# Kernel tuning notes

Hardware: AMD Instinct MI355X
Metric: run time of the kernel (lower is better)

The kernel has to match this reference:

```python
import jax, jax.numpy as jnp
import numpy as np

HIDDEN = 4096
INTER = 11008
BATCH, SEQ = 2, 2048


def _ternary(key, shape):
    # BitNet b1.58 ternary weights in {-1, 0, +1}
    return jax.random.randint(key, shape, -1, 2).astype(jnp.float32)


def setup_inputs() -> dict:
    key = jax.random.key(0)
    kx, kg, ku, kd = jax.random.split(key, 4)
    x = jax.random.normal(kx, (BATCH, SEQ, HIDDEN), dtype=jnp.float32)
    gate_w = _ternary(kg, (INTER, HIDDEN))
    up_w = _ternary(ku, (INTER, HIDDEN))
    down_w = _ternary(kd, (HIDDEN, INTER))
    # per-tensor absmean scales (dequant factors)
    gate_scale = jnp.float32(0.02)
    up_scale = jnp.float32(0.02)
    down_scale = jnp.float32(0.02)
    return {"x": x, "gate_w": gate_w, "up_w": up_w, "down_w": down_w,
            "gate_scale": gate_scale, "up_scale": up_scale, "down_scale": down_scale}


def reference(x, gate_w, up_w, down_w, gate_scale, up_scale, down_scale):
    # QuantizedLinear: y = (x @ W_q^T) * scale, W_q ternary, bias=False
    gate = jnp.einsum('bsh,ih->bsi', x, gate_w) * gate_scale
    up = jnp.einsum('bsh,ih->bsi', x, up_w) * up_scale
    inter = jax.nn.silu(gate) * up  # SwiGLU
    out = jnp.einsum('bsi,hi->bsh', inter, down_w) * down_scale
    return out
```

## Files before the change

### kernel.cpp

```cpp
#include <hip/hip_runtime.h>


typedef short short8 __attribute__((ext_vector_type(8)));
typedef float f32x4 __attribute__((ext_vector_type(4)));
typedef float fvec4 __attribute__((ext_vector_type(4)));
typedef unsigned short usvec4 __attribute__((ext_vector_type(4)));

__device__ __forceinline__ unsigned short f2bf(float f) {
    unsigned int u = __float_as_uint(f);
    u += 0x7FFFu + ((u >> 16) & 1u);
    return (unsigned short)(u >> 16);
}

__global__ void cvt_f32_bf16(const fvec4* __restrict__ src,
                             usvec4* __restrict__ dst, long n4) {
    long i = (long)blockIdx.x * blockDim.x + threadIdx.x;
    if (i < n4) {
        fvec4 v = __builtin_nontemporal_load(src + i);
        usvec4 o;
        o.x = f2bf(v.x); o.y = f2bf(v.y); o.z = f2bf(v.z); o.w = f2bf(v.w);
        dst[i] = o;
    }
}

__global__ void cvt2_f32_bf16_ilv(const fvec4* __restrict__ s0,
                                  const fvec4* __restrict__ s1,
                                  usvec4* __restrict__ d, long n4) {
    long i = (long)blockIdx.x * blockDim.x + threadIdx.x;
    if (i < n4) {
        long j = i >> 10;
        long c = i & 1023;
        long Rg = ((j & ~15L) << 1) | (j & 15);
        fvec4 a = __builtin_nontemporal_load(s0 + i);
        fvec4 b = __builtin_nontemporal_load(s1 + i);
        usvec4 oa, ob;
        oa.x = f2bf(a.x); oa.y = f2bf(a.y); oa.z = f2bf(a.z); oa.w = f2bf(a.w);
        ob.x = f2bf(b.x); ob.y = f2bf(b.y); ob.z = f2bf(b.z); ob.w = f2bf(b.w);
        d[Rg * 1024 + c] = oa;
        d[(Rg + 16) * 1024 + c] = ob;
    }
}

#define GLOBAL_TO_LDS(gp, lp)                                                  \
    __builtin_amdgcn_global_load_lds(                                          \
        (__attribute__((address_space(1))) const void*)(gp),                   \
        (__attribute__((address_space(3))) void*)(lp), 16, 0, 0)

#define BAR() __builtin_amdgcn_s_barrier()
#define SCHEDB() __builtin_amdgcn_sched_barrier(0)
#define LGKM0() do { asm volatile("s_waitcnt lgkmcnt(0)" ::: "memory"); SCHEDB(); } while (0)
#define VMW(n) asm volatile("s_waitcnt vmcnt(" #n ")" ::: "memory")

__device__ __forceinline__ void remap_block(int gy, int& bx, int& by) {
    int nwg = gy << 4;
    int orig = blockIdx.y * 16 + blockIdx.x;
    int q = nwg >> 3, r = nwg & 7;
    int xcd = orig & 7, lid = orig >> 3;
    int wg = (xcd < r ? xcd * (q + 1) : r * (q + 1) + (xcd - r) * q) + lid;
    bx = wg & 15;
    by = wg >> 4;
}

__global__ __launch_bounds__(512, 2)
void gemm1_swiglu(const unsigned short* __restrict__ Xb,
                  const unsigned short* __restrict__ Wc,
                  unsigned short* __restrict__ inter,
                  const float* __restrict__ gs_p,
                  const float* __restrict__ us_p,
                  int K, int I, int n0, int gy) {
    extern __shared__ unsigned short lds[];

    int bx, by;
    remap_block(gy, bx, by);

    const int t = threadIdx.x;
    const int lane = t & 63;
    const int wid = t >> 6;
    const int wm = (wid >> 2) * 128;
    const int wn = (wid & 3) * 64;
    const int fr = lane & 15;
    const int ca = (((lane >> 4) ^ ((fr >> 1) & 3)) << 3);

    const int m_base = bx * 256;
    const long b_row0 = (long)by * 256;

    const int colsw = (((t & 3) ^ ((t >> 3) & 3)) << 3);
    const unsigned short* pa0 = Xb + (size_t)(m_base + (t >> 2)) * K + colsw;
    const unsigned short* pa1 = pa0 + (size_t)128 * K;
    const unsigned short* pb0 = Wc + (size_t)(b_row0 + (t >> 2)) * K + colsw;
    const unsigned short* pb1 = pb0 + (size_t)128 * K;

    f32x4 acc[8][4];
    const f32x4 z = {0.0f, 0.0f, 0.0f, 0.0f};
#pragma unroll
    for (int i = 0; i < 8; ++i)
#pragma unroll
        for (int j = 0; j < 4; ++j) acc[i][j] = z;

    const int aoff = (wm + fr) * 32 + ca;
    const int boff = (wn + fr) * 32 + ca;
    const int Kt = K >> 5;

#pragma unroll
    for (int s = 0; s < 3; ++s) {
        unsigned short* Aq = lds + s * 8192;
        unsigned short* Bq = lds + 32768 + s * 8192;
        GLOBAL_TO_LDS(pa0, Aq + t * 8);
        GLOBAL_TO_LDS(pa1, Aq + 4096 + t * 8);
        GLOBAL_TO_LDS(pb0, Bq + t * 8);
        GLOBAL_TO_LDS(pb1, Bq + 4096 + t * 8);
        pa0 += 32; pa1 += 32; pb0 += 32; pb1 += 32;
    }
    VMW(8);
    BAR();

    auto KT = [&](int q, int pq, bool pf) {
        unsigned short* Aq = lds + q * 8192;
        unsigned short* Bq = lds + 32768 + q * 8192;
        unsigned short* Ap = lds + pq * 8192;
        unsigned short* Bp = lds + 32768 + pq * 8192;
        short8 af[4], bf[4];
#pragma unroll
        for (int i = 0; i < 4; ++i)
            af[i] = *(const short8*)(Aq + aoff + i * 512);
#pragma unroll
        for (int n = 0; n < 4; ++n)
            bf[n] = *(const short8*)(Bq + boff + n * 512);
        if (pf) {
            GLOBAL_TO_LDS(pa0, Ap + t * 8);
            GLOBAL_TO_LDS(pa1, Ap + 4096 + t * 8);
        }
        SCHEDB(); BAR(); LGKM0();
        __builtin_amdgcn_s_setprio(1);
#pragma unroll
        for (int mi = 0; mi < 4; ++mi)
#pragma unroll
            for (int ni = 0; ni < 4; ++ni)
                acc[mi][ni] = __builtin_amdgcn_mfma_f32_16x16x32_bf16(
                    af[mi], bf[ni], acc[mi][ni], 0, 0, 0);
        __builtin_amdgcn_s_setprio(0);
        SCHEDB(); BAR();
#pragma unroll
        for (int i = 0; i < 4; ++i)
            af[i] = *(const short8*)(Aq + aoff + (4 + i) * 512);
        if (pf) {
            GLOBAL_TO_LDS(pb0, Bp + t * 8);
            GLOBAL_TO_LDS(pb1, Bp + 4096 + t * 8);
            pa0 += 32; pa1 += 32; pb0 += 32; pb1 += 32;
        }
        SCHEDB(); BAR(); LGKM0();
        __builtin_amdgcn_s_setprio(1);
#pragma unroll
        for (int mi = 0; mi < 4; ++mi)
#pragma unroll
            for (int ni = 0; ni < 4; ++ni)
                acc[4 + mi][ni] = __builtin_amdgcn_mfma_f32_16x16x32_bf16(
                    af[mi], bf[ni], acc[4 + mi][ni], 0, 0, 0);
        __builtin_amdgcn_s_setprio(0);
    };

    int kt = 0;
    for (; kt < Kt - 3; ++kt) {
        KT(kt & 3, (kt + 3) & 3, true);
        VMW(8);
        BAR();
    }
    KT(kt & 3, 0, false); VMW(4); BAR(); ++kt;
    KT(kt & 3, 0, false); VMW(0); BAR(); ++kt;
    KT(kt & 3, 0, false);

    const float gsc = *gs_p;
    const float usc = *us_p;
    const int row0 = m_base + wm + ((lane >> 4) << 2);
    const int col0 = n0 + by * 128 + (wn >> 1) + fr;
#pragma unroll
    for (int mi = 0; mi < 8; ++mi)
#pragma unroll
        for (int p = 0; p < 2; ++p)
#pragma unroll
            for (int r = 0; r < 4; ++r) {
                float g = acc[mi][2 * p][r] * gsc;
                float u = acc[mi][2 * p + 1][r] * usc;
                float s = g / (1.0f + __expf(-g));
                inter[(size_t)(row0 + mi * 16 + r) * I + (col0 + p * 16)] =
                    f2bf(s * u);
            }
}

__global__ __launch_bounds__(512, 2)
void gemm2_down(const unsigned short* __restrict__ Ab,
                const unsigned short* __restrict__ Dw,
                float* __restrict__ out,
                const float* __restrict__ ds_p,
                int K, int H, int h0, int gy) {
    extern __shared__ unsigned short lds[];

    int bx, by;
    remap_block(gy, bx, by);

    const int t = threadIdx.x;
    const int lane = t & 63;
    const int wid = t >> 6;
    const int wm = (wid >> 2) * 128;
    const int wn = (wid & 3) * 64;
    const int fr = lane & 15;
    const int ca = (((lane >> 4) ^ ((fr >> 1) & 3)) << 3);

    const int m_base = bx * 256;
    const long b_row0 = (long)by * 256;

    const int colsw = (((t & 3) ^ ((t >> 3) & 3)) << 3);
    const unsigned short* pa0 = Ab + (size_t)(m_base + (t >> 2)) * K + colsw;
    const unsigned short* pa1 = pa0 + (size_t)128 * K;
    const unsigned short* pb0 = Dw + (size_t)(b_row0 + (t >> 2)) * K + colsw;
    const unsigned short* pb1 = pb0 + (size_t)128 * K;

    f32x4 acc[8][4];
    const f32x4 z = {0.0f, 0.0f, 0.0f, 0.0f};
#pragma unroll
    for (int i = 0; i < 8; ++i)
#pragma unroll
        for (int j = 0; j < 4; ++j) acc[i][j] = z;

    const int aoff = (wm + fr) * 32 + ca;
    const int boff = (wn + fr) * 32 + ca;
    const int Kt = K >> 5;

#pragma unroll
    for (int s = 0; s < 3; ++s) {
        unsigned short* Aq = lds + s * 8192;
        unsigned short* Bq = lds + 32768 + s * 8192;
        GLOBAL_TO_LDS(pa0, Aq + t * 8);
        GLOBAL_TO_LDS(pa1, Aq + 4096 + t * 8);
        GLOBAL_TO_LDS(pb0, Bq + t * 8);
        GLOBAL_TO_LDS(pb1, Bq + 4096 + t * 8);
        pa0 += 32; pa1 += 32; pb0 += 32; pb1 += 32;
    }
    VMW(8);
    BAR();

    auto KT = [&](int q, int pq, bool pf) {
        unsigned short* Aq = lds + q * 8192;
        unsigned short* Bq = lds + 32768 + q * 8192;
        unsigned short* Ap = lds + pq * 8192;
        unsigned short* Bp = lds + 32768 + pq * 8192;
        short8 af[4], bf[4];
#pragma unroll
        for (int i = 0; i < 4; ++i)
            af[i] = *(const short8*)(Aq + aoff + i * 512);
#pragma unroll
        for (int n = 0; n < 4; ++n)
            bf[n] = *(const short8*)(Bq + boff + n * 512);
        if (pf) {
            GLOBAL_TO_LDS(pa0, Ap + t * 8);
            GLOBAL_TO_LDS(pa1, Ap + 4096 + t * 8);
        }
        SCHEDB(); BAR(); LGKM0();
        __builtin_amdgcn_s_setprio(1);
#pragma unroll
        for (int mi = 0; mi < 4; ++mi)
#pragma unroll
            for (int ni = 0; ni < 4; ++ni)
                acc[mi][ni] = __builtin_amdgcn_mfma_f32_16x16x32_bf16(
                    af[mi], bf[ni], acc[mi][ni], 0, 0, 0);
        __builtin_amdgcn_s_setprio(0);
        SCHEDB(); BAR();
#pragma unroll
        for (int i = 0; i < 4; ++i)
            af[i] = *(const short8*)(Aq + aoff + (4 + i) * 512);
        if (pf) {
            GLOBAL_TO_LDS(pb0, Bp + t * 8);
            GLOBAL_TO_LDS(pb1, Bp + 4096 + t * 8);
            pa0 += 32; pa1 += 32; pb0 += 32; pb1 += 32;
        }
        SCHEDB(); BAR(); LGKM0();
        __builtin_amdgcn_s_setprio(1);
#pragma unroll
        for (int mi = 0; mi < 4; ++mi)
#pragma unroll
            for (int ni = 0; ni < 4; ++ni)
                acc[4 + mi][ni] = __builtin_amdgcn_mfma_f32_16x16x32_bf16(
                    af[mi], bf[ni], acc[4 + mi][ni], 0, 0, 0);
        __builtin_amdgcn_s_setprio(0);
    };

    int kt = 0;
    for (; kt < Kt - 3; ++kt) {
        KT(kt & 3, (kt + 3) & 3, true);
        VMW(8);
        BAR();
    }
    KT(kt & 3, 0, false); VMW(4); BAR(); ++kt;
    KT(kt & 3, 0, false); VMW(0); BAR(); ++kt;
    KT(kt & 3, 0, false);

    const float dsc = *ds_p;
    const int row0 = m_base + wm + ((lane >> 4) << 2);
    const int col0 = h0 + by * 256 + wn + fr;
#pragma unroll
    for (int mi = 0; mi < 8; ++mi)
#pragma unroll
        for (int ni = 0; ni < 4; ++ni)
#pragma unroll
            for (int r = 0; r < 4; ++r)
                out[(size_t)(row0 + mi * 16 + r) * H + (col0 + ni * 16)] =
                    acc[mi][ni][r] * dsc;
}

extern "C" void kernel_launch(void* const* d_in, const int* in_sizes, int n_in,
                              void* d_out, int out_size, void* d_ws, size_t ws_size,
                              hipStream_t stream) {
    (void)in_sizes; (void)n_in; (void)out_size;
    const float* x  = (const float*)d_in[0];
    const float* gw = (const float*)d_in[1];
    const float* uw = (const float*)d_in[2];
    const float* dw = (const float*)d_in[3];
    const float* gs = (const float*)d_in[4];
    const float* us = (const float*)d_in[5];
    const float* ds = (const float*)d_in[6];
    float* out = (float*)d_out;

    const long M = 4096;
    const long Kh = 4096;
    const long I = 11008;
    const long H = 4096;

    (void)hipFuncSetAttribute(reinterpret_cast<const void*>(gemm1_swiglu),
                              hipFuncAttributeMaxDynamicSharedMemorySize, 131072);
    (void)hipFuncSetAttribute(reinterpret_cast<const void*>(gemm2_down),
                              hipFuncAttributeMaxDynamicSharedMemorySize, 131072);

    char* ws = (char*)d_ws;
    unsigned short* Xb = (unsigned short*)ws;
    unsigned short* inter = (unsigned short*)(ws + M * Kh * 2);
    const size_t used = (size_t)M * Kh * 2 + (size_t)M * I * 2;
    if (ws_size < used + 2 * (size_t)256 * I * 2) return;
    char* wbuf = ws + used;
    const size_t avail = ws_size - used;

    {
        long n4 = M * Kh / 4;
        cvt_f32_bf16<<<dim3((unsigned)((n4 + 255) / 256)), dim3(256), 0, stream>>>(
            (const fvec4*)x, (usvec4*)Xb, n4);
    }

    long mr1 = (long)(avail / ((size_t)2 * Kh * 2));
    mr1 = (mr1 / 128) * 128;
    if (mr1 > I) mr1 = I;
    if (mr1 < 128) mr1 = 128;
    unsigned short* Wc = (unsigned short*)wbuf;
    for (long n0 = 0; n0 < I; n0 += mr1) {
        long rc = (I - n0 < mr1) ? (I - n0) : mr1;
        long e4 = rc * Kh / 4;
        unsigned cb = (unsigned)((e4 + 255) / 256);
        cvt2_f32_bf16_ilv<<<dim3(cb), dim3(256), 0, stream>>>(
            (const fvec4*)(gw + n0 * Kh), (const fvec4*)(uw + n0 * Kh),
            (usvec4*)Wc, e4);
        unsigned gy = (unsigned)(rc / 128);
        gemm1_swiglu<<<dim3(16, gy), dim3(512), 131072, stream>>>(
            Xb, Wc, inter, gs, us, (int)Kh, (int)I, (int)n0, (int)gy);
    }

    long mr2 = (long)(avail / ((size_t)I * 2));
    mr2 = (mr2 / 256) * 256;
    if (mr2 > H) mr2 = H;
    if (mr2 < 256) mr2 = 256;
    unsigned short* Wd = (unsigned short*)wbuf;
    for (long h0 = 0; h0 < H; h0 += mr2) {
        long rc = (H - h0 < mr2) ? (H - h0) : mr2;
        long e4 = rc * I / 4;
        unsigned cb = (unsigned)((e4 + 255) / 256);
        cvt_f32_bf16<<<dim3(cb), dim3(256), 0, stream>>>(
            (const fvec4*)(dw + h0 * I), (usvec4*)Wd, e4);
        unsigned gy = (unsigned)(rc / 256);
        gemm2_down<<<dim3(16, gy), dim3(512), 131072, stream>>>(
            inter, Wd, out, ds, (int)I, (int)H, (int)h0, (int)gy);
    }
}
```

Baseline: 1.427 ms.

## Fuse fp32-to-bf16 weight conversion into GEMM B-operand loads via registers

Drops the separate weight conversion kernels and chunked launches. Each GEMM now reads fp32 weights straight from global memory into registers, truncates them to bf16 and writes them into swizzled LDS, interleaving the gate and up rows on the fly. The main loop is restructured into a software pipeline with three A stages filled by direct-to-LDS loads and three register-staged B stages, with MFMA of the previous half overlapping the next loads. This removes the extra global write and re-read of converted weights, but each GEMM block now reads twice as many B bytes and truncates rather than rounds, which is exact for ternary weights.

```diff
diff --git a/kernel.cpp b/kernel.cpp
--- a/kernel.cpp
+++ b/kernel.cpp
@@ -5,6 +5,8 @@
 typedef float f32x4 __attribute__((ext_vector_type(4)));
 typedef float fvec4 __attribute__((ext_vector_type(4)));
 typedef unsigned short usvec4 __attribute__((ext_vector_type(4)));
+typedef unsigned int u32x4 __attribute__((ext_vector_type(4)));
+typedef unsigned int u32x2 __attribute__((ext_vector_type(2)));
 
 __device__ __forceinline__ unsigned short f2bf(float f) {
     unsigned int u = __float_as_uint(f);
@@ -23,24 +25,6 @@
     }
 }
 
-__global__ void cvt2_f32_bf16_ilv(const fvec4* __restrict__ s0,
-                                  const fvec4* __restrict__ s1,
-                                  usvec4* __restrict__ d, long n4) {
-    long i = (long)blockIdx.x * blockDim.x + threadIdx.x;
-    if (i < n4) {
-        long j = i >> 10;
-        long c = i & 1023;
-        long Rg = ((j & ~15L) << 1) | (j & 15);
-        fvec4 a = __builtin_nontemporal_load(s0 + i);
-        fvec4 b = __builtin_nontemporal_load(s1 + i);
-        usvec4 oa, ob;
-        oa.x = f2bf(a.x); oa.y = f2bf(a.y); oa.z = f2bf(a.z); oa.w = f2bf(a.w);
-        ob.x = f2bf(b.x); ob.y = f2bf(b.y); ob.z = f2bf(b.z); ob.w = f2bf(b.w);
-        d[Rg * 1024 + c] = oa;
-        d[(Rg + 16) * 1024 + c] = ob;
-    }
-}
-
 #define GLOBAL_TO_LDS(gp, lp)                                                  \
     __builtin_amdgcn_global_load_lds(                                          \
         (__attribute__((address_space(1))) const void*)(gp),                   \
@@ -49,7 +33,8 @@
 #define BAR() __builtin_amdgcn_s_barrier()
 #define SCHEDB() __builtin_amdgcn_sched_barrier(0)
 #define LGKM0() do { asm volatile("s_waitcnt lgkmcnt(0)" ::: "memory"); SCHEDB(); } while (0)
-#define VMW(n) asm volatile("s_waitcnt vmcnt(" #n ")" ::: "memory")
+#define VMW_(n) asm volatile("s_waitcnt vmcnt(" #n ")" ::: "memory")
+#define VMW(n) VMW_(n)
 
 __device__ __forceinline__ void remap_block(int gy, int& bx, int& by) {
     int nwg = gy << 4;
@@ -61,13 +46,118 @@
     by = wg >> 4;
 }
 
+#define KBODY(BC, BP, DO_PREV, DO_SA, DO_SB, VMTOK, DO_WR)                    \
+  do {                                                                        \
+    BAR();                                                                    \
+    if (DO_SB) {                                                              \
+      _Pragma("unroll") for (int j = 0; j < 4; ++j) {                         \
+        wreg[j] = *(const u32x4*)pb[j];                                       \
+        pb[j] += 32;                                                          \
+      }                                                                       \
+    }                                                                         \
+    {                                                                         \
+      const unsigned short* Aq = lds + qr * 8192;                             \
+      const unsigned short* Bq = lds + 24576 + br * 8192;                     \
+      _Pragma("unroll") for (int i = 0; i < 4; ++i)                           \
+        ah0[i] = *(const short8*)(Aq + aoff + i * 512);                       \
+      _Pragma("unroll") for (int n = 0; n < 4; ++n)                           \
+        BC[n] = *(const short8*)(Bq + boff + n * 512);                        \
+      SCHEDB();                                                               \
+      if (DO_PREV) {                                                          \
+        __builtin_amdgcn_s_setprio(1);                                        \
+        _Pragma("unroll") for (int mi = 0; mi < 4; ++mi)                      \
+          _Pragma("unroll") for (int ni = 0; ni < 4; ++ni)                    \
+            acc[4 + mi][ni] = __builtin_amdgcn_mfma_f32_16x16x32_bf16(        \
+                ah1[mi], BP[ni], acc[4 + mi][ni], 0, 0, 0);                   \
+        __builtin_amdgcn_s_setprio(0);                                        \
+      }                                                                       \
+      SCHEDB();                                                               \
+      if (DO_SA) {                                                            \
+        unsigned short* As = lds + qs * 8192;                                 \
+        GLOBAL_TO_LDS(pa0, As + t * 8);                                       \
+        GLOBAL_TO_LDS(pa1, As + 4096 + t * 8);                                \
+        pa0 += 32; pa1 += 32;                                                 \
+      }                                                                       \
+      SCHEDB();                                                               \
+      LGKM0();                                                                \
+      _Pragma("unroll") for (int i = 0; i < 4; ++i)                           \
+        ah1[i] = *(const short8*)(Aq + aoff + (4 + i) * 512);                 \
+      SCHEDB();                                                               \
+      __builtin_amdgcn_s_setprio(1);                                          \
+      _Pragma("unroll") for (int mi = 0; mi < 4; ++mi)                        \
+        _Pragma("unroll") for (int ni = 0; ni < 4; ++ni)                      \
+          acc[mi][ni] = __builtin_amdgcn_mfma_f32_16x16x32_bf16(              \
+              ah0[mi], BC[ni], acc[mi][ni], 0, 0, 0);                         \
+      __builtin_amdgcn_s_setprio(0);                                          \
+      SCHEDB();                                                               \
+      VMW(VMTOK);                                                             \
+      if (DO_WR) {                                                            \
+        unsigned short* Bw = lds + 24576 + bw * 8192;                         \
+        _Pragma("unroll") for (int j = 0; j < 4; ++j) {                       \
+          unsigned u0 = (wreg[j].x >> 16) | (wreg[j].y & 0xFFFF0000u);        \
+          unsigned u1 = (wreg[j].z >> 16) | (wreg[j].w & 0xFFFF0000u);        \
+          *(u32x2*)(Bw + j * 2048 + wds) = (u32x2){u0, u1};                   \
+        }                                                                     \
+      }                                                                       \
+      LGKM0();                                                                \
+    }                                                                         \
+    qr = qr == 2 ? 0 : qr + 1;                                                \
+    qs = qs == 2 ? 0 : qs + 1;                                                \
+    br = br == 2 ? 0 : br + 1;                                                \
+    bw = bw == 2 ? 0 : bw + 1;                                                \
+  } while (0)
+
+#define KPROLOGUE()                                                           \
+  do {                                                                        \
+    _Pragma("unroll") for (int j = 0; j < 4; ++j) {                           \
+      wreg[j] = *(const u32x4*)pb[j];                                         \
+      pb[j] += 32;                                                            \
+    }                                                                         \
+    GLOBAL_TO_LDS(pa0, lds + t * 8);                                          \
+    GLOBAL_TO_LDS(pa1, lds + 4096 + t * 8);                                   \
+    pa0 += 32; pa1 += 32;                                                     \
+    GLOBAL_TO_LDS(pa0, lds + 8192 + t * 8);                                   \
+    GLOBAL_TO_LDS(pa1, lds + 8192 + 4096 + t * 8);                            \
+    pa0 += 32; pa1 += 32;                                                     \
+    VMW(4);                                \
+    {                                                                         \
+      unsigned short* Bw = lds + 24576;                                       \
+      _Pragma("unroll") for (int j = 0; j < 4; ++j) {                         \
+        unsigned u0 = (wreg[j].x >> 16) | (wreg[j].y & 0xFFFF0000u);          \
+        unsigned u1 = (wreg[j].z >> 16) | (wreg[j].w & 0xFFFF0000u);          \
+        *(u32x2*)(Bw + j * 2048 + wds) = (u32x2){u0, u1};                     \
+      }                                                                       \
+    }                                                                         \
+    VMW(2);                                        \
+    LGKM0();                                                                  \
+  } while (0)
+
+#define KLOOP()                                                               \
+  do {                                                                        \
+    KBODY(bF0, bF1, 0, 1, 1, 2, 1);                                 \
+    KBODY(bF1, bF0, 1, 1, 1, 2, 1);                                 \
+    for (int kt = 2; kt < Kt - 2; kt += 2) {                                  \
+      KBODY(bF0, bF1, 1, 1, 1, 2, 1);                                         \
+      KBODY(bF1, bF0, 1, 1, 1, 2, 1);                                         \
+    }                                                                         \
+    KBODY(bF0, bF1, 1, 0, 1, 0, 1);           \
+    KBODY(bF1, bF0, 1, 0, 0, 0, 0);                   \
+    __builtin_amdgcn_s_setprio(1);                                            \
+    _Pragma("unroll") for (int mi = 0; mi < 4; ++mi)                          \
+      _Pragma("unroll") for (int ni = 0; ni < 4; ++ni)                        \
+        acc[4 + mi][ni] = __builtin_amdgcn_mfma_f32_16x16x32_bf16(            \
+            ah1[mi], bF1[ni], acc[4 + mi][ni], 0, 0, 0);                      \
+    __builtin_amdgcn_s_setprio(0);                                            \
+  } while (0)
+
 __global__ __launch_bounds__(512, 2)
 void gemm1_swiglu(const unsigned short* __restrict__ Xb,
-                  const unsigned short* __restrict__ Wc,
+                  const float* __restrict__ Gw,
+                  const float* __restrict__ Uw,
                   unsigned short* __restrict__ inter,
                   const float* __restrict__ gs_p,
                   const float* __restrict__ us_p,
-                  int K, int I, int n0, int gy) {
+                  int K, int I, int gy) {
     extern __shared__ unsigned short lds[];
 
     int bx, by;
@@ -82,13 +172,23 @@
     const int ca = (((lane >> 4) ^ ((fr >> 1) & 3)) << 3);
 
     const int m_base = bx * 256;
-    const long b_row0 = (long)by * 256;
 
     const int colsw = (((t & 3) ^ ((t >> 3) & 3)) << 3);
     const unsigned short* pa0 = Xb + (size_t)(m_base + (t >> 2)) * K + colsw;
     const unsigned short* pa1 = pa0 + (size_t)128 * K;
-    const unsigned short* pb0 = Wc + (size_t)(b_row0 + (t >> 2)) * K + colsw;
-    const unsigned short* pb1 = pb0 + (size_t)128 * K;
+
+    const float* pb[4];
+#pragma unroll
+    for (int j = 0; j < 4; ++j) {
+        int rl = 64 * j + (t >> 3);
+        int cg = by * 256 + rl;
+        const float* base = ((cg >> 4) & 1) ? Uw : Gw;
+        int srow = ((cg >> 5) << 4) + (cg & 15);
+        pb[j] = base + (size_t)srow * K + 4 * (t & 7);
+    }
+    const int tt = t >> 3;
+    const int pg = ((t >> 1) & 3) ^ ((tt >> 1) & 3);
+    const int wds = tt * 32 + pg * 8 + (t & 1) * 4;
 
     f32x4 acc[8][4];
     const f32x4 z = {0.0f, 0.0f, 0.0f, 0.0f};
@@ -101,78 +201,17 @@
     const int boff = (wn + fr) * 32 + ca;
     const int Kt = K >> 5;
 
-#pragma unroll
-    for (int s = 0; s < 3; ++s) {
-        unsigned short* Aq = lds + s * 8192;
-        unsigned short* Bq = lds + 32768 + s * 8192;
-        GLOBAL_TO_LDS(pa0, Aq + t * 8);
-        GLOBAL_TO_LDS(pa1, Aq + 4096 + t * 8);
-        GLOBAL_TO_LDS(pb0, Bq + t * 8);
-        GLOBAL_TO_LDS(pb1, Bq + 4096 + t * 8);
-        pa0 += 32; pa1 += 32; pb0 += 32; pb1 += 32;
-    }
-    VMW(8);
-    BAR();
-
-    auto KT = [&](int q, int pq, bool pf) {
-        unsigned short* Aq = lds + q * 8192;
-        unsigned short* Bq = lds + 32768 + q * 8192;
-        unsigned short* Ap = lds + pq * 8192;
-        unsigned short* Bp = lds + 32768 + pq * 8192;
-        short8 af[4], bf[4];
-#pragma unroll
-        for (int i = 0; i < 4; ++i)
-            af[i] = *(const short8*)(Aq + aoff + i * 512);
-#pragma unroll
-        for (int n = 0; n < 4; ++n)
-            bf[n] = *(const short8*)(Bq + boff + n * 512);
-        if (pf) {
-            GLOBAL_TO_LDS(pa0, Ap + t * 8);
-            GLOBAL_TO_LDS(pa1, Ap + 4096 + t * 8);
-        }
-        SCHEDB(); BAR(); LGKM0();
-        __builtin_amdgcn_s_setprio(1);
-#pragma unroll
-        for (int mi = 0; mi < 4; ++mi)
-#pragma unroll
-            for (int ni = 0; ni < 4; ++ni)
-                acc[mi][ni] = __builtin_amdgcn_mfma_f32_16x16x32_bf16(
-                    af[mi], bf[ni], acc[mi][ni], 0, 0, 0);
-        __builtin_amdgcn_s_setprio(0);
-        SCHEDB(); BAR();
-#pragma unroll
-        for (int i = 0; i < 4; ++i)
-            af[i] = *(const short8*)(Aq + aoff + (4 + i) * 512);
-        if (pf) {
-            GLOBAL_TO_LDS(pb0, Bp + t * 8);
-            GLOBAL_TO_LDS(pb1, Bp + 4096 + t * 8);
-            pa0 += 32; pa1 += 32; pb0 += 32; pb1 += 32;
-        }
-        SCHEDB(); BAR(); LGKM0();
-        __builtin_amdgcn_s_setprio(1);
-#pragma unroll
-        for (int mi = 0; mi < 4; ++mi)
-#pragma unroll
-            for (int ni = 0; ni < 4; ++ni)
-                acc[4 + mi][ni] = __builtin_amdgcn_mfma_f32_16x16x32_bf16(
-                    af[mi], bf[ni], acc[4 + mi][ni], 0, 0, 0);
-        __builtin_amdgcn_s_setprio(0);
-    };
-
-    int kt = 0;
-    for (; kt < Kt - 3; ++kt) {
-        KT(kt & 3, (kt + 3) & 3, true);
-        VMW(8);
-        BAR();
-    }
-    KT(kt & 3, 0, false); VMW(4); BAR(); ++kt;
-    KT(kt & 3, 0, false); VMW(0); BAR(); ++kt;
-    KT(kt & 3, 0, false);
+    short8 ah0[4], ah1[4], bF0[4], bF1[4];
+    u32x4 wreg[4];
+    int qr = 0, qs = 2, br = 0, bw = 1;
+
+    KPROLOGUE();
+    KLOOP();
 
     const float gsc = *gs_p;
     const float usc = *us_p;
     const int row0 = m_base + wm + ((lane >> 4) << 2);
-    const int col0 = n0 + by * 128 + (wn >> 1) + fr;
+    const int col0 = by * 128 + (wn >> 1) + fr;
 #pragma unroll
     for (int mi = 0; mi < 8; ++mi)
 #pragma unroll
@@ -189,10 +228,10 @@
 
 __global__ __launch_bounds__(512, 2)
 void gemm2_down(const unsigned short* __restrict__ Ab,
-                const unsigned short* __restrict__ Dw,
+                const float* __restrict__ Dw,
                 float* __restrict__ out,
                 const float* __restrict__ ds_p,
-                int K, int H, int h0, int gy) {
+                int K, int H, int gy) {
     extern __shared__ unsigned short lds[];
 
     int bx, by;
@@ -207,13 +246,20 @@
     const int ca = (((lane >> 4) ^ ((fr >> 1) & 3)) << 3);
 
     const int m_base = bx * 256;
-    const long b_row0 = (long)by * 256;
 
     const int colsw = (((t & 3) ^ ((t >> 3) & 3)) << 3);
     const unsigned short* pa0 = Ab + (size_t)(m_base + (t >> 2)) * K + colsw;
     const unsigned short* pa1 = pa0 + (size_t)128 * K;
-    const unsigned short* pb0 = Dw + (size_t)(b_row0 + (t >> 2)) * K + colsw;
-    const unsigned short* pb1 = pb0 + (size_t)128 * K;
+
+    const float* pb[4];
+#pragma unroll
+    for (int j = 0; j < 4; ++j) {
+        int rl = 64 * j + (t >> 3);
+        pb[j] = Dw + (size_t)(by * 256 + rl) * K + 4 * (t & 7);
+    }
+    const int tt = t >> 3;
+    const int pg = ((t >> 1) & 3) ^ ((tt >> 1) & 3);
+    const int wds = tt * 32 + pg * 8 + (t & 1) * 4;
 
     f32x4 acc[8][4];
     const f32x4 z = {0.0f, 0.0f, 0.0f, 0.0f};
@@ -226,77 +272,16 @@
     const int boff = (wn + fr) * 32 + ca;
     const int Kt = K >> 5;
 
-#pragma unroll
-    for (int s = 0; s < 3; ++s) {
-        unsigned short* Aq = lds + s * 8192;
-        unsigned short* Bq = lds + 32768 + s * 8192;
-        GLOBAL_TO_LDS(pa0, Aq + t * 8);
-        GLOBAL_TO_LDS(pa1, Aq + 4096 + t * 8);
-        GLOBAL_TO_LDS(pb0, Bq + t * 8);
-        GLOBAL_TO_LDS(pb1, Bq + 4096 + t * 8);
-        pa0 += 32; pa1 += 32; pb0 += 32; pb1 += 32;
-    }
-    VMW(8);
-    BAR();
-
-    auto KT = [&](int q, int pq, bool pf) {
-        unsigned short* Aq = lds + q * 8192;
-        unsigned short* Bq = lds + 32768 + q * 8192;
-        unsigned short* Ap = lds + pq * 8192;
-        unsigned short* Bp = lds + 32768 + pq * 8192;
-        short8 af[4], bf[4];
-#pragma unroll
-        for (int i = 0; i < 4; ++i)
-            af[i] = *(const short8*)(Aq + aoff + i * 512);
-#pragma unroll
-        for (int n = 0; n < 4; ++n)
-            bf[n] = *(const short8*)(Bq + boff + n * 512);
-        if (pf) {
-            GLOBAL_TO_LDS(pa0, Ap + t * 8);
-            GLOBAL_TO_LDS(pa1, Ap + 4096 + t * 8);
-        }
-        SCHEDB(); BAR(); LGKM0();
-        __builtin_amdgcn_s_setprio(1);
-#pragma unroll
-        for (int mi = 0; mi < 4; ++mi)
-#pragma unroll
-            for (int ni = 0; ni < 4; ++ni)
-                acc[mi][ni] = __builtin_amdgcn_mfma_f32_16x16x32_bf16(
-                    af[mi], bf[ni], acc[mi][ni], 0, 0, 0);
-        __builtin_amdgcn_s_setprio(0);
-        SCHEDB(); BAR();
-#pragma unroll
-        for (int i = 0; i < 4; ++i)
-            af[i] = *(const short8*)(Aq + aoff + (4 + i) * 512);
-        if (pf) {
-            GLOBAL_TO_LDS(pb0, Bp + t * 8);
-            GLOBAL_TO_LDS(pb1, Bp + 4096 + t * 8);
-            pa0 += 32; pa1 += 32; pb0 += 32; pb1 += 32;
-        }
-        SCHEDB(); BAR(); LGKM0();
-        __builtin_amdgcn_s_setprio(1);
-#pragma unroll
-        for (int mi = 0; mi < 4; ++mi)
-#pragma unroll
-            for (int ni = 0; ni < 4; ++ni)
-                acc[4 + mi][ni] = __builtin_amdgcn_mfma_f32_16x16x32_bf16(
-                    af[mi], bf[ni], acc[4 + mi][ni], 0, 0, 0);
-        __builtin_amdgcn_s_setprio(0);
-    };
-
-    int kt = 0;
-    for (; kt < Kt - 3; ++kt) {
-        KT(kt & 3, (kt + 3) & 3, true);
-        VMW(8);
-        BAR();
-    }
-    KT(kt & 3, 0, false); VMW(4); BAR(); ++kt;
-    KT(kt & 3, 0, false); VMW(0); BAR(); ++kt;
-    KT(kt & 3, 0, false);
+    short8 ah0[4], ah1[4], bF0[4], bF1[4];
+    u32x4 wreg[4];
+    int qr = 0, qs = 2, br = 0, bw = 1;
+
+    KPROLOGUE();
+    KLOOP();
 
     const float dsc = *ds_p;
     const int row0 = m_base + wm + ((lane >> 4) << 2);
-    const int col0 = h0 + by * 256 + wn + fr;
+    const int col0 = by * 256 + wn + fr;
 #pragma unroll
     for (int mi = 0; mi < 8; ++mi)
 #pragma unroll
@@ -326,17 +311,15 @@
     const long H = 4096;
 
     (void)hipFuncSetAttribute(reinterpret_cast<const void*>(gemm1_swiglu),
-                              hipFuncAttributeMaxDynamicSharedMemorySize, 131072);
+                              hipFuncAttributeMaxDynamicSharedMemorySize, 98304);
     (void)hipFuncSetAttribute(reinterpret_cast<const void*>(gemm2_down),
-                              hipFuncAttributeMaxDynamicSharedMemorySize, 131072);
+                              hipFuncAttributeMaxDynamicSharedMemorySize, 98304);
 
     char* ws = (char*)d_ws;
     unsigned short* Xb = (unsigned short*)ws;
     unsigned short* inter = (unsigned short*)(ws + M * Kh * 2);
     const size_t used = (size_t)M * Kh * 2 + (size_t)M * I * 2;
-    if (ws_size < used + 2 * (size_t)256 * I * 2) return;
-    char* wbuf = ws + used;
-    const size_t avail = ws_size - used;
+    if (ws_size < used) return;
 
     {
         long n4 = M * Kh / 4;
@@ -344,36 +327,9 @@
             (const fvec4*)x, (usvec4*)Xb, n4);
     }
 
-    long mr1 = (long)(avail / ((size_t)2 * Kh * 2));
-    mr1 = (mr1 / 128) * 128;
-    if (mr1 > I) mr1 = I;
-    if (mr1 < 128) mr1 = 128;
-    unsigned short* Wc = (unsigned short*)wbuf;
-    for (long n0 = 0; n0 < I; n0 += mr1) {
-        long rc = (I - n0 < mr1) ? (I - n0) : mr1;
-        long e4 = rc * Kh / 4;
-        unsigned cb = (unsigned)((e4 + 255) / 256);
-        cvt2_f32_bf16_ilv<<<dim3(cb), dim3(256), 0, stream>>>(
-            (const fvec4*)(gw + n0 * Kh), (const fvec4*)(uw + n0 * Kh),
-            (usvec4*)Wc, e4);
-        unsigned gy = (unsigned)(rc / 128);
-        gemm1_swiglu<<<dim3(16, gy), dim3(512), 131072, stream>>>(
-            Xb, Wc, inter, gs, us, (int)Kh, (int)I, (int)n0, (int)gy);
-    }
-
-    long mr2 = (long)(avail / ((size_t)I * 2));
-    mr2 = (mr2 / 256) * 256;
-    if (mr2 > H) mr2 = H;
-    if (mr2 < 256) mr2 = 256;
-    unsigned short* Wd = (unsigned short*)wbuf;
-    for (long h0 = 0; h0 < H; h0 += mr2) {
-        long rc = (H - h0 < mr2) ? (H - h0) : mr2;
-        long e4 = rc * I / 4;
-        unsigned cb = (unsigned)((e4 + 255) / 256);
-        cvt_f32_bf16<<<dim3(cb), dim3(256), 0, stream>>>(
-            (const fvec4*)(dw + h0 * I), (usvec4*)Wd, e4);
-        unsigned gy = (unsigned)(rc / 256);
-        gemm2_down<<<dim3(16, gy), dim3(512), 131072, stream>>>(
-            inter, Wd, out, ds, (int)I, (int)H, (int)h0, (int)gy);
-    }
-}
+    gemm1_swiglu<<<dim3(16, 86), dim3(512), 98304, stream>>>(
+        Xb, gw, uw, inter, gs, us, (int)Kh, (int)I, 86);
+
+    gemm2_down<<<dim3(16, 16), dim3(512), 98304, stream>>>(
+        inter, dw, out, ds, (int)I, (int)H, 16);
+}
```

New measurement: 1.870 ms. +31.1%, slower.

## Software-pipeline LDS fragment reads across k-tiles with register double-buffering

Applied to the files above, without the earlier changes.

Restructures the main k-loop of both GEMMs so the A/B fragments for the next k-tile are read from LDS into registers (double-buffered B fragments, split A halves) while the current tile's MFMAs run. Partial lgkmcnt waits replace full waits, and all four global-to-LDS prefetches for a stage are issued together. This cuts the per-iteration barriers from three to one, aiming to hide LDS latency and synchronisation overhead behind MFMA work. It also slightly relaxes the workspace size check. The cost is more live registers and a schedule that is more fragile with respect to wait counts.

```diff
diff --git a/kernel.cpp b/kernel.cpp
--- a/kernel.cpp
+++ b/kernel.cpp
@@ -48,7 +48,7 @@
 
 #define BAR() __builtin_amdgcn_s_barrier()
 #define SCHEDB() __builtin_amdgcn_sched_barrier(0)
-#define LGKM0() do { asm volatile("s_waitcnt lgkmcnt(0)" ::: "memory"); SCHEDB(); } while (0)
+#define LGKM(n) do { asm volatile("s_waitcnt lgkmcnt(" #n ")" ::: "memory"); SCHEDB(); } while (0)
 #define VMW(n) asm volatile("s_waitcnt vmcnt(" #n ")" ::: "memory")
 
 __device__ __forceinline__ void remap_block(int gy, int& bx, int& by) {
@@ -61,6 +61,85 @@
     by = wg >> 4;
 }
 
+#define KITER(KT_, BFC, BFN, TOK4, PF_, RA_)                                   \
+  do {                                                                         \
+    LGKM(4);                        \
+    __builtin_amdgcn_s_setprio(1);                                             \
+    _Pragma("unroll") for (int mi = 0; mi < 4; ++mi)                           \
+      _Pragma("unroll") for (int ni = 0; ni < 4; ++ni)                         \
+        acc[mi][ni] = __builtin_amdgcn_mfma_f32_16x16x32_bf16(                 \
+            ah0[mi], BFC[ni], acc[mi][ni], 0, 0, 0);                           \
+    __builtin_amdgcn_s_setprio(0);                                             \
+    SCHEDB();                                                                  \
+    if (TOK4) { VMW(4); } else { VMW(0); }                                     \
+    BAR();                                   \
+    if (RA_) {                                                                 \
+      const unsigned short* Aq = lds + ((((KT_) + 1) & 3) << 13);              \
+      const unsigned short* Bq = lds + 32768 + ((((KT_) + 1) & 3) << 13);      \
+      _Pragma("unroll") for (int i = 0; i < 4; ++i)                            \
+        ah0[i] = *(const short8*)(Aq + aoff + i * 512);                        \
+      _Pragma("unroll") for (int n = 0; n < 4; ++n)                            \
+        BFN[n] = *(const short8*)(Bq + boff + n * 512);                        \
+    }                                                                          \
+    if (PF_) {                                                                 \
+      unsigned short* Aw = lds + ((((KT_) + 3) & 3) << 13);                    \
+      unsigned short* Bw = lds + 32768 + ((((KT_) + 3) & 3) << 13);            \
+      GLOBAL_TO_LDS(pa0, Aw + t * 8);                                          \
+      GLOBAL_TO_LDS(pa1, Aw + 4096 + t * 8);                                   \
+      GLOBAL_TO_LDS(pb0, Bw + t * 8);                                          \
+      GLOBAL_TO_LDS(pb1, Bw + 4096 + t * 8);                                   \
+      pa0 += 32; pa1 += 32; pb0 += 32; pb1 += 32;                              \
+    }                                                                          \
+    SCHEDB();                                                                  \
+    if (RA_) { LGKM(8); } else { LGKM(0); }   \
+    __builtin_amdgcn_s_setprio(1);                                             \
+    _Pragma("unroll") for (int mi = 0; mi < 4; ++mi)                           \
+      _Pragma("unroll") for (int ni = 0; ni < 4; ++ni)                         \
+        acc[4 + mi][ni] = __builtin_amdgcn_mfma_f32_16x16x32_bf16(             \
+            ah1[mi], BFC[ni], acc[4 + mi][ni], 0, 0, 0);                       \
+    __builtin_amdgcn_s_setprio(0);                                             \
+    SCHEDB();                                                                  \
+    if (RA_) {          \
+      const unsigned short* Aq = lds + ((((KT_) + 1) & 3) << 13);              \
+      _Pragma("unroll") for (int i = 0; i < 4; ++i)                            \
+        ah1[i] = *(const short8*)(Aq + aoff + (4 + i) * 512);                  \
+      SCHEDB();                                                                \
+    }                                                                          \
+  } while (0)
+
+#define KPRO()                                                                 \
+  do {                                                                         \
+    _Pragma("unroll") for (int s = 0; s < 3; ++s) {                            \
+      unsigned short* Aw = lds + (s << 13);                                    \
+      unsigned short* Bw = lds + 32768 + (s << 13);                            \
+      GLOBAL_TO_LDS(pa0, Aw + t * 8);                                          \
+      GLOBAL_TO_LDS(pa1, Aw + 4096 + t * 8);                                   \
+      GLOBAL_TO_LDS(pb0, Bw + t * 8);                                          \
+      GLOBAL_TO_LDS(pb1, Bw + 4096 + t * 8);                                   \
+      pa0 += 32; pa1 += 32; pb0 += 32; pb1 += 32;                              \
+    }                                                                          \
+    VMW(8); BAR();                     \
+    _Pragma("unroll") for (int i = 0; i < 4; ++i)                              \
+      ah0[i] = *(const short8*)(lds + aoff + i * 512);                         \
+    _Pragma("unroll") for (int n = 0; n < 4; ++n)                              \
+      bfA[n] = *(const short8*)(lds + 32768 + boff + n * 512);                 \
+    _Pragma("unroll") for (int i = 0; i < 4; ++i)                              \
+      ah1[i] = *(const short8*)(lds + aoff + (4 + i) * 512);                   \
+    SCHEDB();                                                                  \
+  } while (0)
+
+#define KLOOP()                                                                \
+  do {                                                                         \
+    for (int kt = 0; kt < Kt - 4; kt += 2) {                                   \
+      KITER(kt, bfA, bfB, 1, 1, 1);                                            \
+      KITER(kt + 1, bfB, bfA, 1, 1, 1);                                        \
+    }                                                                          \
+    KITER(Kt - 4, bfA, bfB, 1, 1, 1);                                          \
+    KITER(Kt - 3, bfB, bfA, 1, 0, 1);                                          \
+    KITER(Kt - 2, bfA, bfB, 0, 0, 1);                                          \
+    KITER(Kt - 1, bfB, bfA, 0, 0, 0);                                          \
+  } while (0)
+
 __global__ __launch_bounds__(512, 2)
 void gemm1_swiglu(const unsigned short* __restrict__ Xb,
                   const unsigned short* __restrict__ Wc,
@@ -101,73 +180,10 @@
     const int boff = (wn + fr) * 32 + ca;
     const int Kt = K >> 5;
 
-#pragma unroll
-    for (int s = 0; s < 3; ++s) {
-        unsigned short* Aq = lds + s * 8192;
-        unsigned short* Bq = lds + 32768 + s * 8192;
-        GLOBAL_TO_LDS(pa0, Aq + t * 8);
-        GLOBAL_TO_LDS(pa1, Aq + 4096 + t * 8);
-        GLOBAL_TO_LDS(pb0, Bq + t * 8);
-        GLOBAL_TO_LDS(pb1, Bq + 4096 + t * 8);
-        pa0 += 32; pa1 += 32; pb0 += 32; pb1 += 32;
-    }
-    VMW(8);
-    BAR();
-
-    auto KT = [&](int q, int pq, bool pf) {
-        unsigned short* Aq = lds + q * 8192;
-        unsigned short* Bq = lds + 32768 + q * 8192;
-        unsigned short* Ap = lds + pq * 8192;
-        unsigned short* Bp = lds + 32768 + pq * 8192;
-        short8 af[4], bf[4];
-#pragma unroll
-        for (int i = 0; i < 4; ++i)
-            af[i] = *(const short8*)(Aq + aoff + i * 512);
-#pragma unroll
-        for (int n = 0; n < 4; ++n)
-            bf[n] = *(const short8*)(Bq + boff + n * 512);
-        if (pf) {
-            GLOBAL_TO_LDS(pa0, Ap + t * 8);
-            GLOBAL_TO_LDS(pa1, Ap + 4096 + t * 8);
-        }
-        SCHEDB(); BAR(); LGKM0();
-        __builtin_amdgcn_s_setprio(1);
-#pragma unroll
-        for (int mi = 0; mi < 4; ++mi)
-#pragma unroll
-            for (int ni = 0; ni < 4; ++ni)
-                acc[mi][ni] = __builtin_amdgcn_mfma_f32_16x16x32_bf16(
-                    af[mi], bf[ni], acc[mi][ni], 0, 0, 0);
-        __builtin_amdgcn_s_setprio(0);
-        SCHEDB(); BAR();
-#pragma unroll
-        for (int i = 0; i < 4; ++i)
-            af[i] = *(const short8*)(Aq + aoff + (4 + i) * 512);
-        if (pf) {
-            GLOBAL_TO_LDS(pb0, Bp + t * 8);
-            GLOBAL_TO_LDS(pb1, Bp + 4096 + t * 8);
-            pa0 += 32; pa1 += 32; pb0 += 32; pb1 += 32;
-        }
-        SCHEDB(); BAR(); LGKM0();
-        __builtin_amdgcn_s_setprio(1);
-#pragma unroll
-        for (int mi = 0; mi < 4; ++mi)
-#pragma unroll
-            for (int ni = 0; ni < 4; ++ni)
-                acc[4 + mi][ni] = __builtin_amdgcn_mfma_f32_16x16x32_bf16(
-                    af[mi], bf[ni], acc[4 + mi][ni], 0, 0, 0);
-        __builtin_amdgcn_s_setprio(0);
-    };
-
-    int kt = 0;
-    for (; kt < Kt - 3; ++kt) {
-        KT(kt & 3, (kt + 3) & 3, true);
-        VMW(8);
-        BAR();
-    }
-    KT(kt & 3, 0, false); VMW(4); BAR(); ++kt;
-    KT(kt & 3, 0, false); VMW(0); BAR(); ++kt;
-    KT(kt & 3, 0, false);
+    short8 ah0[4], ah1[4], bfA[4], bfB[4];
+
+    KPRO();
+    KLOOP();
 
     const float gsc = *gs_p;
     const float usc = *us_p;
@@ -192,7 +208,7 @@
                 const unsigned short* __restrict__ Dw,
                 float* __restrict__ out,
                 const float* __restrict__ ds_p,
-                int K, int H, int h0, int gy) {
+                int K, int H, int n0, int gy) {
     extern __shared__ unsigned short lds[];
 
     int bx, by;
@@ -226,77 +242,14 @@
     const int boff = (wn + fr) * 32 + ca;
     const int Kt = K >> 5;
 
-#pragma unroll
-    for (int s = 0; s < 3; ++s) {
-        unsigned short* Aq = lds + s * 8192;
-        unsigned short* Bq = lds + 32768 + s * 8192;
-        GLOBAL_TO_LDS(pa0, Aq + t * 8);
-        GLOBAL_TO_LDS(pa1, Aq + 4096 + t * 8);
-        GLOBAL_TO_LDS(pb0, Bq + t * 8);
-        GLOBAL_TO_LDS(pb1, Bq + 4096 + t * 8);
-        pa0 += 32; pa1 += 32; pb0 += 32; pb1 += 32;
-    }
-    VMW(8);
-    BAR();
-
-    auto KT = [&](int q, int pq, bool pf) {
-        unsigned short* Aq = lds + q * 8192;
-        unsigned short* Bq = lds + 32768 + q * 8192;
-        unsigned short* Ap = lds + pq * 8192;
-        unsigned short* Bp = lds + 32768 + pq * 8192;
-        short8 af[4], bf[4];
-#pragma unroll
-        for (int i = 0; i < 4; ++i)
-            af[i] = *(const short8*)(Aq + aoff + i * 512);
-#pragma unroll
-        for (int n = 0; n < 4; ++n)
-            bf[n] = *(const short8*)(Bq + boff + n * 512);
-        if (pf) {
-            GLOBAL_TO_LDS(pa0, Ap + t * 8);
-            GLOBAL_TO_LDS(pa1, Ap + 4096 + t * 8);
-        }
-        SCHEDB(); BAR(); LGKM0();
-        __builtin_amdgcn_s_setprio(1);
-#pragma unroll
-        for (int mi = 0; mi < 4; ++mi)
-#pragma unroll
-            for (int ni = 0; ni < 4; ++ni)
-                acc[mi][ni] = __builtin_amdgcn_mfma_f32_16x16x32_bf16(
-                    af[mi], bf[ni], acc[mi][ni], 0, 0, 0);
-        __builtin_amdgcn_s_setprio(0);
-        SCHEDB(); BAR();
-#pragma unroll
-        for (int i = 0; i < 4; ++i)
-            af[i] = *(const short8*)(Aq + aoff + (4 + i) * 512);
-        if (pf) {
-            GLOBAL_TO_LDS(pb0, Bp + t * 8);
-            GLOBAL_TO_LDS(pb1, Bp + 4096 + t * 8);
-            pa0 += 32; pa1 += 32; pb0 += 32; pb1 += 32;
-        }
-        SCHEDB(); BAR(); LGKM0();
-        __builtin_amdgcn_s_setprio(1);
-#pragma unroll
-        for (int mi = 0; mi < 4; ++mi)
-#pragma unroll
-            for (int ni = 0; ni < 4; ++ni)
-                acc[4 + mi][ni] = __builtin_amdgcn_mfma_f32_16x16x32_bf16(
-                    af[mi], bf[ni], acc[4 + mi][ni], 0, 0, 0);
-        __builtin_amdgcn_s_setprio(0);
-    };
-
-    int kt = 0;
-    for (; kt < Kt - 3; ++kt) {
-        KT(kt & 3, (kt + 3) & 3, true);
-        VMW(8);
-        BAR();
-    }
-    KT(kt & 3, 0, false); VMW(4); BAR(); ++kt;
-    KT(kt & 3, 0, false); VMW(0); BAR(); ++kt;
-    KT(kt & 3, 0, false);
+    short8 ah0[4], ah1[4], bfA[4], bfB[4];
+
+    KPRO();
+    KLOOP();
 
     const float dsc = *ds_p;
     const int row0 = m_base + wm + ((lane >> 4) << 2);
-    const int col0 = h0 + by * 256 + wn + fr;
+    const int col0 = n0 + by * 256 + wn + fr;
 #pragma unroll
     for (int mi = 0; mi < 8; ++mi)
 #pragma unroll
@@ -334,7 +287,7 @@
     unsigned short* Xb = (unsigned short*)ws;
     unsigned short* inter = (unsigned short*)(ws + M * Kh * 2);
     const size_t used = (size_t)M * Kh * 2 + (size_t)M * I * 2;
-    if (ws_size < used + 2 * (size_t)256 * I * 2) return;
+    if (ws_size < used + 2 * (size_t)256 * Kh * 2) return;
     char* wbuf = ws + used;
     const size_t avail = ws_size - used;
 
```

New measurement: 1.394 ms. 2.3% less time.
